# Kernel optimization log

Hardware: AMD Instinct MI355X
Metric: run time of the kernel (lower is better)

## Reference

```python
import jax, jax.numpy as jnp
import numpy as np

GAMMA = 0.1   # permanent impact coef
ETA = 0.3     # temporary impact coef
B = 2_000_000
FEATURE_DIM = 32
HIDDEN = 64


def setup_inputs() -> dict:
    key = jax.random.key(0)
    k_os, k_liq, k_w1, k_b1, k_w2, k_b2 = jax.random.split(key, 6)
    order_sizes = jax.random.normal(k_os, (B,), dtype=jnp.float32) * 500.0
    # liquidity must be positive (used under sqrt and as divisor); scale ~ market_depth=1000
    liquidity = jax.random.uniform(k_liq, (B,), dtype=jnp.float32) * 1000.0 + 100.0
    # encoder params: Linear(3,64) -> ReLU -> Linear(64,32) -> LayerNorm(32)
    lim1 = 1.0 / np.sqrt(3.0)
    lim2 = 1.0 / np.sqrt(HIDDEN)
    W1 = jax.random.uniform(k_w1, (3, HIDDEN), dtype=jnp.float32, minval=-lim1, maxval=lim1)
    b1 = jax.random.uniform(k_b1, (HIDDEN,), dtype=jnp.float32, minval=-lim1, maxval=lim1)
    W2 = jax.random.uniform(k_w2, (HIDDEN, FEATURE_DIM), dtype=jnp.float32, minval=-lim2, maxval=lim2)
    b2 = jax.random.uniform(k_b2, (FEATURE_DIM,), dtype=jnp.float32, minval=-lim2, maxval=lim2)
    ln_w = jnp.ones((FEATURE_DIM,), dtype=jnp.float32)
    ln_b = jnp.zeros((FEATURE_DIM,), dtype=jnp.float32)
    return {"order_sizes": order_sizes, "liquidity": liquidity,
            "W1": W1, "b1": b1, "W2": W2, "b2": b2, "ln_w": ln_w, "ln_b": ln_b}


def _layernorm(x, w, b, eps=1e-5):
    mu = jnp.mean(x, axis=-1, keepdims=True)
    var = jnp.var(x, axis=-1, keepdims=True)
    return (x - mu) * jax.lax.rsqrt(var + eps) * w + b


def reference(order_sizes, liquidity, W1, b1, W2, b2, ln_w, ln_b):
    # vectorized replacement of the per-element .item() loop
    perm = GAMMA * order_sizes / liquidity                                   # [B]
    temp = ETA * jnp.sign(order_sizes) * jnp.sqrt(jnp.abs(order_sizes)) / jnp.sqrt(liquidity)  # [B]
    total = perm + temp                                                      # [B]
    feats = jnp.stack([perm, temp, total], axis=1)                           # [B, 3]
    h = jax.nn.relu(feats @ W1 + b1)                                         # [B, 64]
    encoded = _layernorm(h @ W2 + b2, ln_w, ln_b)                            # [B, 32]
    return perm, temp, total, encoded
```

## Files before the change

### kernel.cpp

```cpp
#include <hip/hip_runtime.h>
#include <hip/hip_bf16.h>

#define GAMMA 0.1f
#define ETA   0.3f
#define ITERS 2

typedef __attribute__((ext_vector_type(8))) short short8;
typedef __attribute__((ext_vector_type(4))) float f32x4;

__device__ __forceinline__ short f2bf(float x) {
    unsigned u = __float_as_uint(x);
    u += 0x7FFFu + ((u >> 16) & 1u);
    return (short)(u >> 16);
}

__global__ __launch_bounds__(256) void market_impact_mfma(
    const float* __restrict__ os_g, const float* __restrict__ liq_g,
    const float* __restrict__ W1,  const float* __restrict__ b1g,
    const float* __restrict__ W2,  const float* __restrict__ b2,
    const float* __restrict__ lnw, const float* __restrict__ lnb,
    float* __restrict__ out, int B)
{
    const int tid  = threadIdx.x;
    const int lane = tid & 63;
    const int g    = lane >> 4;
    const int c    = lane & 15;

    float u[16], v[16], bb[16];
    #pragma unroll
    for (int kc = 0; kc < 2; ++kc)
        #pragma unroll
        for (int j = 0; j < 8; ++j) {
            int k = kc * 32 + g * 8 + j;
            float w0 = W1[k], w1 = W1[64 + k], w2r = W1[128 + k];
            u[kc * 8 + j]  = w0 + w2r;
            v[kc * 8 + j]  = w1 + w2r;
            bb[kc * 8 + j] = b1g[k];
        }

    short8 wfrag[2][2];
    #pragma unroll
    for (int kc = 0; kc < 2; ++kc)
        #pragma unroll
        for (int cc = 0; cc < 2; ++cc) {
            short8 t;
            #pragma unroll
            for (int j = 0; j < 8; ++j) {
                int k = kc * 32 + g * 8 + j;
                t[j] = f2bf(W2[k * 32 + cc * 16 + c]);
            }
            wfrag[kc][cc] = t;
        }

    float b2a[8], lnwa[8], lnba[8];
    #pragma unroll
    for (int cc = 0; cc < 2; ++cc) {
        float4 bq = *reinterpret_cast<const float4*>(b2  + cc * 16 + g * 4);
        float4 wq = *reinterpret_cast<const float4*>(lnw + cc * 16 + g * 4);
        float4 bl = *reinterpret_cast<const float4*>(lnb + cc * 16 + g * 4);
        b2a[cc*4+0] = bq.x; b2a[cc*4+1] = bq.y; b2a[cc*4+2] = bq.z; b2a[cc*4+3] = bq.w;
        lnwa[cc*4+0] = wq.x; lnwa[cc*4+1] = wq.y; lnwa[cc*4+2] = wq.z; lnwa[cc*4+3] = wq.w;
        lnba[cc*4+0] = bl.x; lnba[cc*4+1] = bl.y; lnba[cc*4+2] = bl.z; lnba[cc*4+3] = bl.w;
    }

    const long long wid = (long long)blockIdx.x * 4 + (tid >> 6);
    float* enc = out + 3LL * B;

    #pragma unroll 1
    for (int it = 0; it < ITERS; ++it) {
        long long base = (wid * ITERS + it) * 64;
        if (base >= B) break;

        int r  = (int)base + lane;
        bool ok = r < B;
        float o  = ok ? os_g[r]  : 0.f;
        float lq = ok ? liq_g[r] : 1.f;
        float perm = GAMMA * o / lq;
        float temp = ETA * copysignf(sqrtf(fabsf(o)), o) * rsqrtf(lq);
        float tot  = perm + temp;
        if (ok) {
            __builtin_nontemporal_store(perm, &out[r]);
            __builtin_nontemporal_store(temp, &out[B + r]);
            __builtin_nontemporal_store(tot,  &out[2 * B + r]);
        }

        #pragma unroll
        for (int mt = 0; mt < 4; ++mt) {
            float pm = __shfl(perm, mt * 16 + c);
            float tm = __shfl(temp, mt * 16 + c);
            short8 a0, a1;
            #pragma unroll
            for (int j = 0; j < 8; ++j) {
                float h0 = fmaxf(0.f, fmaf(pm, u[j],     fmaf(tm, v[j],     bb[j])));
                float h1 = fmaxf(0.f, fmaf(pm, u[8 + j], fmaf(tm, v[8 + j], bb[8 + j])));
                a0[j] = f2bf(h0);
                a1[j] = f2bf(h1);
            }

            f32x4 d0 = {0.f, 0.f, 0.f, 0.f};
            f32x4 d1 = {0.f, 0.f, 0.f, 0.f};
            d0 = __builtin_amdgcn_mfma_f32_16x16x32_bf16(wfrag[0][0], a0, d0, 0, 0, 0);
            d0 = __builtin_amdgcn_mfma_f32_16x16x32_bf16(wfrag[1][0], a1, d0, 0, 0, 0);
            d1 = __builtin_amdgcn_mfma_f32_16x16x32_bf16(wfrag[0][1], a0, d1, 0, 0, 0);
            d1 = __builtin_amdgcn_mfma_f32_16x16x32_bf16(wfrag[1][1], a1, d1, 0, 0, 0);

            float x[8];
            #pragma unroll
            for (int reg = 0; reg < 4; ++reg) {
                x[reg]     = d0[reg] + b2a[reg];
                x[4 + reg] = d1[reg] + b2a[4 + reg];
            }
            float s = 0.f, q = 0.f;
            #pragma unroll
            for (int j = 0; j < 8; ++j) { s += x[j]; q = fmaf(x[j], x[j], q); }
            s += __shfl_xor(s, 16); s += __shfl_xor(s, 32);
            q += __shfl_xor(q, 16); q += __shfl_xor(q, 32);
            float mu   = s * 0.03125f;
            float var  = fmaf(q, 0.03125f, -mu * mu);
            float rstd = rsqrtf(var + 1e-5f);

            int row = (int)base + mt * 16 + c;
            if (row < B) {
                f32x4 o0, o1;
                o0[0] = fmaf((x[0] - mu) * rstd, lnwa[0], lnba[0]);
                o0[1] = fmaf((x[1] - mu) * rstd, lnwa[1], lnba[1]);
                o0[2] = fmaf((x[2] - mu) * rstd, lnwa[2], lnba[2]);
                o0[3] = fmaf((x[3] - mu) * rstd, lnwa[3], lnba[3]);
                o1[0] = fmaf((x[4] - mu) * rstd, lnwa[4], lnba[4]);
                o1[1] = fmaf((x[5] - mu) * rstd, lnwa[5], lnba[5]);
                o1[2] = fmaf((x[6] - mu) * rstd, lnwa[6], lnba[6]);
                o1[3] = fmaf((x[7] - mu) * rstd, lnwa[7], lnba[7]);
                float* rp = enc + (long long)row * 32;
                __builtin_nontemporal_store(o0, reinterpret_cast<f32x4*>(rp + g * 4));
                __builtin_nontemporal_store(o1, reinterpret_cast<f32x4*>(rp + 16 + g * 4));
            }
        }
    }
}

extern "C" void kernel_launch(void* const* d_in, const int* in_sizes, int n_in,
                              void* d_out, int out_size, void* d_ws, size_t ws_size,
                              hipStream_t stream) {
    const float* os_g = (const float*)d_in[0];
    const float* liq  = (const float*)d_in[1];
    const float* W1   = (const float*)d_in[2];
    const float* b1   = (const float*)d_in[3];
    const float* W2   = (const float*)d_in[4];
    const float* b2   = (const float*)d_in[5];
    const float* lnw  = (const float*)d_in[6];
    const float* lnb  = (const float*)d_in[7];
    float* out = (float*)d_out;
    const int B = in_sizes[0];

    const int rows_per_block = 4 * ITERS * 64;
    const int grid = (B + rows_per_block - 1) / rows_per_block;
    market_impact_mfma<<<grid, 256, 0, stream>>>(
        os_g, liq, W1, b1, W2, b2, lnw, lnb, out, B);
}
```

Before: 86.36 us.

## Split elementwise impact streams into separate vectorized kernel before encoder

Moves the perm/temp/total computation into its own kernel that uses float4 loads and stores. The encoder kernel then reads perm and temp back from the output buffer instead of recomputing them from the inputs. The aim is a cleanly vectorized streaming pass for the three scalar outputs. The cost is a second kernel launch and an extra round trip of 16 bytes per row through global memory, and the data written by the first kernel may already be evicted because of the nontemporal stores.

```diff
diff --git a/kernel.cpp b/kernel.cpp
--- a/kernel.cpp
+++ b/kernel.cpp
@@ -1,5 +1,4 @@
 #include <hip/hip_runtime.h>
-#include <hip/hip_bf16.h>
 
 #define GAMMA 0.1f
 #define ETA   0.3f
@@ -14,8 +13,37 @@
     return (short)(u >> 16);
 }
 
-__global__ __launch_bounds__(256) void market_impact_mfma(
+__global__ __launch_bounds__(256) void elemwise_streams(
     const float* __restrict__ os_g, const float* __restrict__ liq_g,
+    float* __restrict__ out, int B)
+{
+    const int n4 = B >> 2;
+    const int i4 = blockIdx.x * 256 + threadIdx.x;
+    if (i4 < n4) {
+        f32x4 o = reinterpret_cast<const f32x4*>(os_g)[i4];
+        f32x4 l = reinterpret_cast<const f32x4*>(liq_g)[i4];
+        f32x4 p, t, s;
+        #pragma unroll
+        for (int j = 0; j < 4; ++j) {
+            p[j] = GAMMA * o[j] / l[j];
+            t[j] = ETA * copysignf(sqrtf(fabsf(o[j])), o[j]) * rsqrtf(l[j]);
+            s[j] = p[j] + t[j];
+        }
+        __builtin_nontemporal_store(p, reinterpret_cast<f32x4*>(out) + i4);
+        __builtin_nontemporal_store(t, reinterpret_cast<f32x4*>(out + B) + i4);
+        __builtin_nontemporal_store(s, reinterpret_cast<f32x4*>(out + 2LL * B) + i4);
+    }
+    if (blockIdx.x == 0 && threadIdx.x == 0) {
+        for (int r = n4 * 4; r < B; ++r) {
+            float o = os_g[r], l = liq_g[r];
+            float p = GAMMA * o / l;
+            float t = ETA * copysignf(sqrtf(fabsf(o)), o) * rsqrtf(l);
+            out[r] = p; out[B + r] = t; out[2LL * B + r] = p + t;
+        }
+    }
+}
+
+__global__ __launch_bounds__(256) void market_impact_enc(
     const float* __restrict__ W1,  const float* __restrict__ b1g,
     const float* __restrict__ W2,  const float* __restrict__ b2,
     const float* __restrict__ lnw, const float* __restrict__ lnb,
@@ -73,16 +101,8 @@
 
         int r  = (int)base + lane;
         bool ok = r < B;
-        float o  = ok ? os_g[r]  : 0.f;
-        float lq = ok ? liq_g[r] : 1.f;
-        float perm = GAMMA * o / lq;
-        float temp = ETA * copysignf(sqrtf(fabsf(o)), o) * rsqrtf(lq);
-        float tot  = perm + temp;
-        if (ok) {
-            __builtin_nontemporal_store(perm, &out[r]);
-            __builtin_nontemporal_store(temp, &out[B + r]);
-            __builtin_nontemporal_store(tot,  &out[2 * B + r]);
-        }
+        float perm = ok ? out[r]     : 0.f;
+        float temp = ok ? out[B + r] : 0.f;
 
         #pragma unroll
         for (int mt = 0; mt < 4; ++mt) {
@@ -152,8 +172,12 @@
     float* out = (float*)d_out;
     const int B = in_sizes[0];
 
+    const int n4 = B >> 2;
+    const int grid1 = (n4 + 255) / 256;
+    elemwise_streams<<<grid1, 256, 0, stream>>>(os_g, liq, out, B);
+
     const int rows_per_block = 4 * ITERS * 64;
-    const int grid = (B + rows_per_block - 1) / rows_per_block;
-    market_impact_mfma<<<grid, 256, 0, stream>>>(
-        os_g, liq, W1, b1, W2, b2, lnw, lnb, out, B);
+    const int grid2 = (B + rows_per_block - 1) / rows_per_block;
+    market_impact_enc<<<grid2, 256, 0, stream>>>(
+        W1, b1, W2, b2, lnw, lnb, out, B);
 }
```

New measurement: 102.5 us. 18.7% more time.
